# Kernel tuning notes

Measured on AMD Instinct MI355X. Metric: run time of the kernel, lower is better.

Reference implementation:

```python
import jax, jax.numpy as jnp
import numpy as np

B, D, L, Q, E, NB, NI = 32, 16, 512, 8, 128, 30, 100000
BN_EPS = 1e-3  # tf.layers.batch_normalization default epsilon
LO, HI = 0.001, 1.0  # histogram_fixed_width value_range
_BN_INV = 1.0 / np.sqrt(1.0 + BN_EPS)  # inference BN with moving_mean=0, moving_var=1


def _bn(x, g, b):
    return g * (x * np.float32(_BN_INV)) + b


def setup_inputs() -> dict:
    key = jax.random.key(0)
    ks = jax.random.split(key, 16)
    dims = [NB, 128, 64, 32, 1]
    inp = {
        "doc": jax.random.randint(ks[0], (B, D, L), 0, NI, dtype=jnp.int32),
        "query": jax.random.randint(ks[1], (B, Q), 0, NI, dtype=jnp.int32),
        "item_embedding": jax.random.normal(ks[2], (NI, E), dtype=jnp.float32),
        "idf_table": jax.random.uniform(ks[3], (NI, 1), dtype=jnp.float32),
        "w_gate": jax.random.normal(ks[4], (Q,), dtype=jnp.float32),
        "g_in": jnp.ones((NB,), jnp.float32),
        "b_in": jnp.zeros((NB,), jnp.float32),
    }
    for i in range(4):
        fan_in, fan_out = dims[i], dims[i + 1]
        kW = jax.random.fold_in(ks[5], i)
        inp[f"W{i}"] = jax.random.normal(kW, (fan_in, fan_out), dtype=jnp.float32) / np.float32(np.sqrt(fan_in))
        inp[f"b{i}"] = jnp.zeros((fan_out,), jnp.float32)
        inp[f"g{i}"] = jnp.ones((fan_out,), jnp.float32)
        inp[f"be{i}"] = jnp.zeros((fan_out,), jnp.float32)
    return inp


def reference(doc, query, item_embedding, idf_table, w_gate, g_in, b_in,
              W0, b0, g0, be0, W1, b1, g1, be1, W2, b2, g2, be2, W3, b3, g3, be3):
    # Embedding lookups
    doc_vec = item_embedding[doc].reshape(B, D * L, E)      # [B, D*L, E]
    q_vec = item_embedding[query]                            # [B, Q, E]
    q_idf = idf_table[query][..., 0]                         # [B, Q]

    # Term gating network: softmax(w * idf) over query terms
    gate = jax.nn.softmax(w_gate * q_idf, axis=-1)           # [B, Q]

    # Cosine similarity of every doc token vs every query term
    d_norm = jnp.sqrt(jnp.sum(doc_vec * doc_vec, axis=-1))   # [B, D*L]
    q_norm = jnp.sqrt(jnp.sum(q_vec * q_vec, axis=-1))       # [B, Q]
    dots = jnp.einsum('bne,bqe->bqn', doc_vec, q_vec)        # [B, Q, D*L]
    sims = dots / (d_norm[:, None, :] * q_norm[:, :, None] + 1e-8)

    # Matching histogram: tf.histogram_fixed_width([0.001, 1], nbins) semantics
    idx = jnp.clip(jnp.floor((sims - LO) / (HI - LO) * NB).astype(jnp.int32), 0, NB - 1)
    rows = B * Q * D
    flat = (jnp.arange(rows, dtype=jnp.int32)[:, None] * NB + idx.reshape(rows, L)).reshape(-1)
    hist = jax.ops.segment_sum(jnp.ones((rows * L,), jnp.float32), flat,
                               num_segments=rows * NB).reshape(B, Q, D, NB)

    # DeepNet: BN -> [dense -> BN -> tanh] x 4 (dropout off at inference)
    x = _bn(hist, g_in, b_in)
    for W, b, g, be in ((W0, b0, g0, be0), (W1, b1, g1, be1),
                        (W2, b2, g2, be2), (W3, b3, g3, be3)):
        x = jnp.tanh(_bn(x @ W + b, g, be))
    query_out = x[..., 0]                                    # [B, Q, D]

    # Score aggregation over query terms
    return jnp.sum(query_out * gate[:, :, None], axis=1)     # [B, D]
```

## Files before the change

### kernel.cpp

```cpp
#include <hip/hip_runtime.h>
#include <math.h>


#define BN_INV 0.99950037468777346f

__device__ __forceinline__ float shflx(float v, int m) {
    return __shfl_xor(v, m, 64);
}

__device__ __forceinline__ int sel8i(int v0, int v1, int v2, int v3,
                                     int v4, int v5, int v6, int v7, int i) {
    int a0 = (i & 1) ? v1 : v0;
    int a1 = (i & 1) ? v3 : v2;
    int a2 = (i & 1) ? v5 : v4;
    int a3 = (i & 1) ? v7 : v6;
    int b0 = (i & 2) ? a1 : a0;
    int b1 = (i & 2) ? a3 : a2;
    return (i & 4) ? b1 : b0;
}

__device__ __forceinline__ float sel8f(float v0, float v1, float v2, float v3,
                                       float v4, float v5, float v6, float v7, int i) {
    float a0 = (i & 1) ? v1 : v0;
    float a1 = (i & 1) ? v3 : v2;
    float a2 = (i & 1) ? v5 : v4;
    float a3 = (i & 1) ? v7 : v6;
    float b0 = (i & 2) ? a1 : a0;
    float b1 = (i & 2) ? a3 : a2;
    return (i & 4) ? b1 : b0;
}

__device__ __forceinline__ float tanh_fast(float x) {
    float y = fminf(fmaxf(x, -9.0f), 9.0f);
    float t = exp2f(y * 2.8853901817f);
    return (t - 1.0f) * __builtin_amdgcn_rcpf(t + 1.0f);
}

__device__ __forceinline__ float4 ld4(const float* base, int elem_off) {
    return *(const float4*)(base + elem_off);
}

template <bool PARTIAL>
__global__ __launch_bounds__(256, 8)
void drmm_hist(const int* __restrict__ doc,
               const int* __restrict__ query,
               const float* __restrict__ emb,
               float* __restrict__ hist_out)
{
    __shared__ float histw[4][8][32];
    __shared__ float qn_s[8];

    const int tid  = threadIdx.x;
    const int bid  = blockIdx.x;
    const int b    = bid >> 8;
    const int wid  = tid >> 6;
    const int lane = tid & 63;
    const int g    = lane >> 3;
    const int j    = lane & 7;

    for (int i = tid; i < 4 * 8 * 32; i += 256) ((float*)histw)[i] = 0.0f;

    const int* qrow = query + b * 8;
    const int qi0 = __builtin_amdgcn_readfirstlane(qrow[0]);
    const int qi1 = __builtin_amdgcn_readfirstlane(qrow[1]);
    const int qi2 = __builtin_amdgcn_readfirstlane(qrow[2]);
    const int qi3 = __builtin_amdgcn_readfirstlane(qrow[3]);
    const int qi4 = __builtin_amdgcn_readfirstlane(qrow[4]);
    const int qi5 = __builtin_amdgcn_readfirstlane(qrow[5]);
    const int qi6 = __builtin_amdgcn_readfirstlane(qrow[6]);
    const int qi7 = __builtin_amdgcn_readfirstlane(qrow[7]);

    const float* qb0 = emb + (size_t)qi0 * 128;
    const float* qb1 = emb + (size_t)qi1 * 128;
    const float* qb2 = emb + (size_t)qi2 * 128;
    const float* qb3 = emb + (size_t)qi3 * 128;
    const float* qb4 = emb + (size_t)qi4 * 128;
    const float* qb5 = emb + (size_t)qi5 * 128;
    const float* qb6 = emb + (size_t)qi6 * 128;
    const float* qb7 = emb + (size_t)qi7 * 128;

    if (wid == 0) {
        int q = lane >> 3, jj = lane & 7;
        int qis = sel8i(qi0, qi1, qi2, qi3, qi4, qi5, qi6, qi7, q);
        const float4* qq = (const float4*)(emb + (size_t)qis * 128) + jj * 4;
        float s = 0.f;
#pragma unroll
        for (int c = 0; c < 4; ++c) {
            float4 x = qq[c];
            s = fmaf(x.x, x.x, s); s = fmaf(x.y, x.y, s);
            s = fmaf(x.z, x.z, s); s = fmaf(x.w, x.w, s);
        }
        s += shflx(s, 1); s += shflx(s, 2); s += shflx(s, 4);
        if (jj == 0) qn_s[q] = sqrtf(s);
    }
    __syncthreads();

    const int gtok = bid * 32 + wid * 8 + g;
    const int idx  = doc[gtok];
    const float* rbase = emb + (size_t)idx * 128;
    const int eo = j * 4;

    float dd = 0.f;
    float dq0 = 0.f, dq1 = 0.f, dq2 = 0.f, dq3 = 0.f;
    float dq4 = 0.f, dq5 = 0.f, dq6 = 0.f, dq7 = 0.f;

    float4 r0 = ld4(rbase, eo);
    float4 r1 = ld4(rbase, eo + 32);

#define KSTEP(RV, KO) {                                                     \
        const int e = eo + (KO);                                            \
        float4 v  = RV;                                                     \
        float4 a0 = ld4(qb0, e), a1 = ld4(qb1, e);                          \
        float4 a2 = ld4(qb2, e), a3 = ld4(qb3, e);                          \
        float4 a4 = ld4(qb4, e), a5 = ld4(qb5, e);                          \
        float4 a6 = ld4(qb6, e), a7 = ld4(qb7, e);                          \
        dd = fmaf(v.x, v.x, dd); dd = fmaf(v.y, v.y, dd);                   \
        dd = fmaf(v.z, v.z, dd); dd = fmaf(v.w, v.w, dd);                   \
        dq0 = fmaf(v.x, a0.x, dq0); dq0 = fmaf(v.y, a0.y, dq0);             \
        dq0 = fmaf(v.z, a0.z, dq0); dq0 = fmaf(v.w, a0.w, dq0);             \
        dq1 = fmaf(v.x, a1.x, dq1); dq1 = fmaf(v.y, a1.y, dq1);             \
        dq1 = fmaf(v.z, a1.z, dq1); dq1 = fmaf(v.w, a1.w, dq1);             \
        dq2 = fmaf(v.x, a2.x, dq2); dq2 = fmaf(v.y, a2.y, dq2);             \
        dq2 = fmaf(v.z, a2.z, dq2); dq2 = fmaf(v.w, a2.w, dq2);             \
        dq3 = fmaf(v.x, a3.x, dq3); dq3 = fmaf(v.y, a3.y, dq3);             \
        dq3 = fmaf(v.z, a3.z, dq3); dq3 = fmaf(v.w, a3.w, dq3);             \
        dq4 = fmaf(v.x, a4.x, dq4); dq4 = fmaf(v.y, a4.y, dq4);             \
        dq4 = fmaf(v.z, a4.z, dq4); dq4 = fmaf(v.w, a4.w, dq4);             \
        dq5 = fmaf(v.x, a5.x, dq5); dq5 = fmaf(v.y, a5.y, dq5);             \
        dq5 = fmaf(v.z, a5.z, dq5); dq5 = fmaf(v.w, a5.w, dq5);             \
        dq6 = fmaf(v.x, a6.x, dq6); dq6 = fmaf(v.y, a6.y, dq6);             \
        dq6 = fmaf(v.z, a6.z, dq6); dq6 = fmaf(v.w, a6.w, dq6);             \
        dq7 = fmaf(v.x, a7.x, dq7); dq7 = fmaf(v.y, a7.y, dq7);             \
        dq7 = fmaf(v.z, a7.z, dq7); dq7 = fmaf(v.w, a7.w, dq7);             \
    }

    float4 r2 = ld4(rbase, eo + 64);
    KSTEP(r0, 0)
    float4 r3 = ld4(rbase, eo + 96);
    KSTEP(r1, 32)
    KSTEP(r2, 64)
    KSTEP(r3, 96)
#undef KSTEP

#pragma unroll
    for (int off = 1; off <= 4; off <<= 1) {
        dd  += shflx(dd, off);
        dq0 += shflx(dq0, off); dq1 += shflx(dq1, off);
        dq2 += shflx(dq2, off); dq3 += shflx(dq3, off);
        dq4 += shflx(dq4, off); dq5 += shflx(dq5, off);
        dq6 += shflx(dq6, off); dq7 += shflx(dq7, off);
    }

    {
        float dqj = sel8f(dq0, dq1, dq2, dq3, dq4, dq5, dq6, dq7, j);
        float sim = dqj / (sqrtf(dd) * qn_s[j] + 1e-8f);
        float u = (sim - 0.001f) / 0.999f * 30.0f;
        int bin = (int)floorf(u);
        bin = bin < 0 ? 0 : (bin > 29 ? 29 : bin);
        atomicAdd(&histw[wid][j][bin], 1.0f);
    }
    __syncthreads();

    if (tid < 240) {
        int q = tid / 30, k = tid - q * 30;
        float s = histw[0][q][k] + histw[1][q][k]
                + histw[2][q][k] + histw[3][q][k];
        if (PARTIAL) {
            hist_out[(size_t)bid * 240 + tid] = s;
        } else {
            atomicAdd(&hist_out[(bid >> 4) * 240 + tid], s);
        }
    }
}

template <bool PARTIAL>
__global__ __launch_bounds__(512, 4)
void drmm_mlp(const float* __restrict__ hist_g,
              const int* __restrict__ query,
              const float* __restrict__ idf,
              const float* __restrict__ w_gate,
              const float* __restrict__ g_in, const float* __restrict__ b_in,
              const float* __restrict__ W0, const float* __restrict__ b0,
              const float* __restrict__ g0, const float* __restrict__ be0,
              const float* __restrict__ W1, const float* __restrict__ b1,
              const float* __restrict__ g1, const float* __restrict__ be1,
              const float* __restrict__ W2, const float* __restrict__ b2,
              const float* __restrict__ g2, const float* __restrict__ be2,
              const float* __restrict__ W3, const float* __restrict__ b3,
              const float* __restrict__ g3, const float* __restrict__ be3,
              float* __restrict__ out)
{
    __shared__ float xrow[8][30];
    __shared__ float h1s[8][128];
    __shared__ float h2s[8][64];
    __shared__ float h3s[8][32];
    __shared__ float gate_s[8];
    __shared__ float part[8];

    const int tid  = threadIdx.x;
    const int bd   = blockIdx.x;
    const int b    = bd >> 4;
    const int wid  = tid >> 6;
    const int lane = tid & 63;

    if (tid >= 504) {
        int q = tid - 504;
        float z = w_gate[q] * idf[query[b * 8 + q]];
        float m = z;
        m = fmaxf(m, shflx(m, 1)); m = fmaxf(m, shflx(m, 2)); m = fmaxf(m, shflx(m, 4));
        float e = expf(z - m);
        float s = e;
        s += shflx(s, 1); s += shflx(s, 2); s += shflx(s, 4);
        gate_s[q] = e / s;
    }

    if (tid < 240) {
        int q = tid / 30, k = tid - q * 30;
        float s;
        if (PARTIAL) {
            const float* hp = hist_g + (size_t)bd * 16 * 240 + tid;
            float s0 = 0.f;
#pragma unroll
            for (int p = 0; p < 16; ++p) s0 += hp[p * 240];
            s = s0;
        } else {
            s = hist_g[bd * 240 + tid];
        }
        xrow[q][k] = g_in[k] * (s * BN_INV) + b_in[k];
    }
    __syncthreads();

    {
        float a0 = 0.f, a1 = 0.f;
#pragma unroll
        for (int k = 0; k < 30; ++k) {
            float xk = xrow[wid][k];
            a0 += xk * W0[k * 128 + lane];
            a1 += xk * W0[k * 128 + 64 + lane];
        }
        a0 += b0[lane]; a1 += b0[lane + 64];
        h1s[wid][lane]      = tanh_fast(g0[lane]      * (a0 * BN_INV) + be0[lane]);
        h1s[wid][lane + 64] = tanh_fast(g0[lane + 64] * (a1 * BN_INV) + be0[lane + 64]);
    }
    __syncthreads();

    {
        float a = 0.f;
#pragma unroll 8
        for (int k = 0; k < 128; ++k) a += h1s[wid][k] * W1[k * 64 + lane];
        a += b1[lane];
        h2s[wid][lane] = tanh_fast(g1[lane] * (a * BN_INV) + be1[lane]);
    }
    __syncthreads();

    if (lane < 32) {
        float a = 0.f;
#pragma unroll 8
        for (int k = 0; k < 64; ++k) a += h2s[wid][k] * W2[k * 32 + lane];
        a += b2[lane];
        h3s[wid][lane] = tanh_fast(g2[lane] * (a * BN_INV) + be2[lane]);
    }
    __syncthreads();

    if (lane == 0) {
        float a = 0.f;
#pragma unroll
        for (int k = 0; k < 32; ++k) a += h3s[wid][k] * W3[k];
        a += b3[0];
        float y = tanh_fast(g3[0] * (a * BN_INV) + be3[0]);
        part[wid] = gate_s[wid] * y;
    }
    __syncthreads();

    if (tid == 0) {
        float s = 0.f;
#pragma unroll
        for (int q = 0; q < 8; ++q) s += part[q];
        out[bd] = s;
    }
}

extern "C" void kernel_launch(void* const* d_in, const int* in_sizes, int n_in,
                              void* d_out, int out_size, void* d_ws, size_t ws_size,
                              hipStream_t stream) {
    (void)in_sizes; (void)n_in; (void)out_size;
    const int*   doc    = (const int*)d_in[0];
    const int*   query  = (const int*)d_in[1];
    const float* emb    = (const float*)d_in[2];
    const float* idf    = (const float*)d_in[3];
    const float* w_gate = (const float*)d_in[4];
    const float* g_in   = (const float*)d_in[5];
    const float* b_in   = (const float*)d_in[6];
    const float* W0  = (const float*)d_in[7];
    const float* b0  = (const float*)d_in[8];
    const float* g0  = (const float*)d_in[9];
    const float* be0 = (const float*)d_in[10];
    const float* W1  = (const float*)d_in[11];
    const float* b1  = (const float*)d_in[12];
    const float* g1  = (const float*)d_in[13];
    const float* be1 = (const float*)d_in[14];
    const float* W2  = (const float*)d_in[15];
    const float* b2  = (const float*)d_in[16];
    const float* g2  = (const float*)d_in[17];
    const float* be2 = (const float*)d_in[18];
    const float* W3  = (const float*)d_in[19];
    const float* b3  = (const float*)d_in[20];
    const float* g3  = (const float*)d_in[21];
    const float* be3 = (const float*)d_in[22];

    float* hist_g = (float*)d_ws;
    const size_t need_partial = (size_t)8192 * 240 * sizeof(float);

    if (ws_size >= need_partial) {
        drmm_hist<true><<<dim3(8192), dim3(256), 0, stream>>>(doc, query, emb, hist_g);
        drmm_mlp<true><<<dim3(512), dim3(512), 0, stream>>>(
            hist_g, query, idf, w_gate, g_in, b_in,
            W0, b0, g0, be0, W1, b1, g1, be1,
            W2, b2, g2, be2, W3, b3, g3, be3, (float*)d_out);
    } else {
        hipMemsetAsync(hist_g, 0, 512 * 240 * sizeof(float), stream);
        drmm_hist<false><<<dim3(8192), dim3(256), 0, stream>>>(doc, query, emb, hist_g);
        drmm_mlp<false><<<dim3(512), dim3(512), 0, stream>>>(
            hist_g, query, idf, w_gate, g_in, b_in,
            W0, b0, g0, be0, W1, b1, g1, be1,
            W2, b2, g2, be2, W3, b3, g3, be3, (float*)d_out);
    }
}
```

Baseline: 57.68 us.

## Stage query embeddings in LDS, enlarge hist blocks, cache W1 in LDS for MLP

The histogram kernel now runs 512-thread blocks covering 64 tokens each, so the grid is halved. It stages the 8 query embedding rows in shared memory once per block instead of having every lane reload them from global memory. It issues all four doc-row float4 loads up front, with asm pins to keep them in flight, and halves the number of partial histograms the MLP must reduce. The MLP kernel copies W1 into 32KB of LDS and drops one barrier, which adds an up-front copy and LDS pressure and lowers the occupancy hint to 3.

```diff
diff --git a/kernel.cpp b/kernel.cpp
--- a/kernel.cpp
+++ b/kernel.cpp
@@ -40,25 +40,30 @@
     return *(const float4*)(base + elem_off);
 }
 
+#define PIN4(V) asm volatile("" : "+v"((V).x), "+v"((V).y), "+v"((V).z), "+v"((V).w))
+
 template <bool PARTIAL>
-__global__ __launch_bounds__(256, 8)
+__global__ __launch_bounds__(512, 8)
 void drmm_hist(const int* __restrict__ doc,
                const int* __restrict__ query,
                const float* __restrict__ emb,
                float* __restrict__ hist_out)
 {
-    __shared__ float histw[4][8][32];
+    __shared__ float histw[8][8][32];
     __shared__ float qn_s[8];
+    __shared__ float4 qlds[8][32];
 
     const int tid  = threadIdx.x;
     const int bid  = blockIdx.x;
-    const int b    = bid >> 8;
+    const int b    = bid >> 7;
     const int wid  = tid >> 6;
     const int lane = tid & 63;
-    const int g    = lane >> 3;
-    const int j    = lane & 7;
-
-    for (int i = tid; i < 4 * 8 * 32; i += 256) ((float*)histw)[i] = 0.0f;
+    const int j    = tid & 7;
+
+    const int gtok = bid * 64 + (tid >> 3);
+    const int idx  = doc[gtok];
+
+    for (int i = tid; i < 8 * 8 * 32; i += 512) ((float*)histw)[i] = 0.0f;
 
     const int* qrow = query + b * 8;
     const int qi0 = __builtin_amdgcn_readfirstlane(qrow[0]);
@@ -70,50 +75,46 @@
     const int qi6 = __builtin_amdgcn_readfirstlane(qrow[6]);
     const int qi7 = __builtin_amdgcn_readfirstlane(qrow[7]);
 
-    const float* qb0 = emb + (size_t)qi0 * 128;
-    const float* qb1 = emb + (size_t)qi1 * 128;
-    const float* qb2 = emb + (size_t)qi2 * 128;
-    const float* qb3 = emb + (size_t)qi3 * 128;
-    const float* qb4 = emb + (size_t)qi4 * 128;
-    const float* qb5 = emb + (size_t)qi5 * 128;
-    const float* qb6 = emb + (size_t)qi6 * 128;
-    const float* qb7 = emb + (size_t)qi7 * 128;
+    if (tid < 256) {
+        int q = tid >> 5;
+        int c = tid & 31;
+        int qis = sel8i(qi0, qi1, qi2, qi3, qi4, qi5, qi6, qi7, q);
+        qlds[q][c] = *((const float4*)(emb + (size_t)qis * 128) + c);
+    }
+    __syncthreads();
 
     if (wid == 0) {
         int q = lane >> 3, jj = lane & 7;
-        int qis = sel8i(qi0, qi1, qi2, qi3, qi4, qi5, qi6, qi7, q);
-        const float4* qq = (const float4*)(emb + (size_t)qis * 128) + jj * 4;
         float s = 0.f;
 #pragma unroll
         for (int c = 0; c < 4; ++c) {
-            float4 x = qq[c];
+            float4 x = qlds[q][jj * 4 + c];
             s = fmaf(x.x, x.x, s); s = fmaf(x.y, x.y, s);
             s = fmaf(x.z, x.z, s); s = fmaf(x.w, x.w, s);
         }
         s += shflx(s, 1); s += shflx(s, 2); s += shflx(s, 4);
         if (jj == 0) qn_s[q] = sqrtf(s);
     }
-    __syncthreads();
-
-    const int gtok = bid * 32 + wid * 8 + g;
-    const int idx  = doc[gtok];
+
     const float* rbase = emb + (size_t)idx * 128;
     const int eo = j * 4;
+
+    float4 A0 = ld4(rbase, eo);
+    float4 A1 = ld4(rbase, eo + 32);
+    float4 A2 = ld4(rbase, eo + 64);
+    float4 A3 = ld4(rbase, eo + 96);
 
     float dd = 0.f;
     float dq0 = 0.f, dq1 = 0.f, dq2 = 0.f, dq3 = 0.f;
     float dq4 = 0.f, dq5 = 0.f, dq6 = 0.f, dq7 = 0.f;
 
-    float4 r0 = ld4(rbase, eo);
-    float4 r1 = ld4(rbase, eo + 32);
-
-#define KSTEP(RV, KO) {                                                     \
-        const int e = eo + (KO);                                            \
-        float4 v  = RV;                                                     \
-        float4 a0 = ld4(qb0, e), a1 = ld4(qb1, e);                          \
-        float4 a2 = ld4(qb2, e), a3 = ld4(qb3, e);                          \
-        float4 a4 = ld4(qb4, e), a5 = ld4(qb5, e);                          \
-        float4 a6 = ld4(qb6, e), a7 = ld4(qb7, e);                          \
+#define KSTEP(V, K) {                                                       \
+        const int S = (K) * 8 + j;                                          \
+        float4 v  = (V);                                                    \
+        float4 a0 = qlds[0][S], a1 = qlds[1][S];                            \
+        float4 a2 = qlds[2][S], a3 = qlds[3][S];                            \
+        float4 a4 = qlds[4][S], a5 = qlds[5][S];                            \
+        float4 a6 = qlds[6][S], a7 = qlds[7][S];                            \
         dd = fmaf(v.x, v.x, dd); dd = fmaf(v.y, v.y, dd);                   \
         dd = fmaf(v.z, v.z, dd); dd = fmaf(v.w, v.w, dd);                   \
         dq0 = fmaf(v.x, a0.x, dq0); dq0 = fmaf(v.y, a0.y, dq0);             \
@@ -134,12 +135,10 @@
         dq7 = fmaf(v.z, a7.z, dq7); dq7 = fmaf(v.w, a7.w, dq7);             \
     }
 
-    float4 r2 = ld4(rbase, eo + 64);
-    KSTEP(r0, 0)
-    float4 r3 = ld4(rbase, eo + 96);
-    KSTEP(r1, 32)
-    KSTEP(r2, 64)
-    KSTEP(r3, 96)
+    PIN4(A0); KSTEP(A0, 0)
+    PIN4(A1); KSTEP(A1, 1)
+    PIN4(A2); KSTEP(A2, 2)
+    PIN4(A3); KSTEP(A3, 3)
 #undef KSTEP
 
 #pragma unroll
@@ -150,6 +149,8 @@
         dq4 += shflx(dq4, off); dq5 += shflx(dq5, off);
         dq6 += shflx(dq6, off); dq7 += shflx(dq7, off);
     }
+
+    __syncthreads();
 
     {
         float dqj = sel8f(dq0, dq1, dq2, dq3, dq4, dq5, dq6, dq7, j);
@@ -163,18 +164,20 @@
 
     if (tid < 240) {
         int q = tid / 30, k = tid - q * 30;
-        float s = histw[0][q][k] + histw[1][q][k]
-                + histw[2][q][k] + histw[3][q][k];
+        float s = ((histw[0][q][k] + histw[1][q][k])
+                 + (histw[2][q][k] + histw[3][q][k]))
+                + ((histw[4][q][k] + histw[5][q][k])
+                 + (histw[6][q][k] + histw[7][q][k]));
         if (PARTIAL) {
             hist_out[(size_t)bid * 240 + tid] = s;
         } else {
-            atomicAdd(&hist_out[(bid >> 4) * 240 + tid], s);
+            atomicAdd(&hist_out[(bid >> 3) * 240 + tid], s);
         }
     }
 }
 
 template <bool PARTIAL>
-__global__ __launch_bounds__(512, 4)
+__global__ __launch_bounds__(512, 3)
 void drmm_mlp(const float* __restrict__ hist_g,
               const int* __restrict__ query,
               const float* __restrict__ idf,
@@ -190,6 +193,7 @@
               const float* __restrict__ g3, const float* __restrict__ be3,
               float* __restrict__ out)
 {
+    __shared__ float W1l[8192];
     __shared__ float xrow[8][30];
     __shared__ float h1s[8][128];
     __shared__ float h2s[8][64];
@@ -202,6 +206,10 @@
     const int b    = bd >> 4;
     const int wid  = tid >> 6;
     const int lane = tid & 63;
+
+#pragma unroll
+    for (int i = 0; i < 4; ++i)
+        ((float4*)W1l)[tid + i * 512] = ((const float4*)W1)[tid + i * 512];
 
     if (tid >= 504) {
         int q = tid - 504;
@@ -218,11 +226,9 @@
         int q = tid / 30, k = tid - q * 30;
         float s;
         if (PARTIAL) {
-            const float* hp = hist_g + (size_t)bd * 16 * 240 + tid;
-            float s0 = 0.f;
-#pragma unroll
-            for (int p = 0; p < 16; ++p) s0 += hp[p * 240];
-            s = s0;
+            const float* hp = hist_g + (size_t)bd * 8 * 240 + tid;
+            s = ((hp[0] + hp[240]) + (hp[480] + hp[720]))
+              + ((hp[960] + hp[1200]) + (hp[1440] + hp[1680]));
         } else {
             s = hist_g[bd * 240 + tid];
         }
@@ -246,8 +252,8 @@
 
     {
         float a = 0.f;
-#pragma unroll 8
-        for (int k = 0; k < 128; ++k) a += h1s[wid][k] * W1[k * 64 + lane];
+#pragma unroll 16
+        for (int k = 0; k < 128; ++k) a += h1s[wid][k] * W1l[k * 64 + lane];
         a += b1[lane];
         h2s[wid][lane] = tanh_fast(g1[lane] * (a * BN_INV) + be1[lane]);
     }
@@ -260,7 +266,6 @@
         a += b2[lane];
         h3s[wid][lane] = tanh_fast(g2[lane] * (a * BN_INV) + be2[lane]);
     }
-    __syncthreads();
 
     if (lane == 0) {
         float a = 0.f;
@@ -309,17 +314,17 @@
     const float* be3 = (const float*)d_in[22];
 
     float* hist_g = (float*)d_ws;
-    const size_t need_partial = (size_t)8192 * 240 * sizeof(float);
+    const size_t need_partial = (size_t)4096 * 240 * sizeof(float);
 
     if (ws_size >= need_partial) {
-        drmm_hist<true><<<dim3(8192), dim3(256), 0, stream>>>(doc, query, emb, hist_g);
+        drmm_hist<true><<<dim3(4096), dim3(512), 0, stream>>>(doc, query, emb, hist_g);
         drmm_mlp<true><<<dim3(512), dim3(512), 0, stream>>>(
             hist_g, query, idf, w_gate, g_in, b_in,
             W0, b0, g0, be0, W1, b1, g1, be1,
             W2, b2, g2, be2, W3, b3, g3, be3, (float*)d_out);
     } else {
         hipMemsetAsync(hist_g, 0, 512 * 240 * sizeof(float), stream);
-        drmm_hist<false><<<dim3(8192), dim3(256), 0, stream>>>(doc, query, emb, hist_g);
+        drmm_hist<false><<<dim3(4096), dim3(512), 0, stream>>>(doc, query, emb, hist_g);
         drmm_mlp<false><<<dim3(512), dim3(512), 0, stream>>>(
             hist_g, query, idf, w_gate, g_in, b_in,
             W0, b0, g0, be0, W1, b1, g1, be1,
```

Result: faster. 47.98 us (-16.8%).
